# Performance work log

Hardware: AMD Instinct MI355X
Metric: run time of the kernel (lower is better)

## Reference

```python
import jax, jax.numpy as jnp
import numpy as np

MOLS = 64
ATOMS = 256
N = MOLS * ATOMS
K_GB = 32
K_GNN = 16
HID = 128
OFFSET = 0.009            # GB dielectric offset (nm)
ALPHA, BETA, GAMMA = 1.0, 0.8, 4.85  # OBC2 coefficients
EPS_FACTOR = 138.935456   # Coulomb constant, kJ*nm/(mol*e^2)
PREF = -EPS_FACTOR * (1.0 - 1.0 / 78.5)


def _edges(key, k_neigh):
    # random intra-molecule neighbors, no self loops (mimics radius-graph structure)
    src = jnp.repeat(jnp.arange(N), k_neigh)
    off = jax.random.randint(key, (N * k_neigh,), 1, ATOMS)
    dst = (src // ATOMS) * ATOMS + (src % ATOMS + off) % ATOMS
    return jnp.stack([src, dst]).astype(jnp.int32)


def setup_inputs() -> dict:
    key = jax.random.key(0)
    ks = jax.random.split(key, 8)
    pos = (jax.random.uniform(ks[0], (N, 3), jnp.float32) * 1.5)
    q = jax.random.uniform(ks[1], (N, 1), jnp.float32) - 0.5
    rad = 0.15 + 0.05 * jax.random.uniform(ks[2], (N, 1), jnp.float32)
    scl = 0.8 + 0.2 * jax.random.uniform(ks[3], (N, 1), jnp.float32)
    rest = jax.random.uniform(ks[4], (N, 4), jnp.float32)
    atom_features = jnp.concatenate([q, rad, scl, rest], axis=1)
    batch = jnp.repeat(jnp.arange(MOLS), ATOMS).astype(jnp.int32)
    edge_index = _edges(ks[5], K_GB)
    gnn_edge_index = _edges(ks[6], K_GNN)

    def lin(k, fi, fo):
        return (jax.random.normal(k, (fi, fo), jnp.float32) / np.float32(np.sqrt(fi)),
                jnp.zeros((fo,), jnp.float32))
    kw = jax.random.split(ks[7], 6)
    i1_w1, i1_b1 = lin(kw[0], 2 * 2 + 1, HID)
    i1_w2, i1_b2 = lin(kw[1], HID, HID)
    i2_w1, i2_b1 = lin(kw[2], 2 * HID + 1, HID)
    i2_w2, i2_b2 = lin(kw[3], HID, HID)
    i3_w1, i3_b1 = lin(kw[4], 2 * HID + 1, HID)
    i3_w2, i3_b2 = lin(kw[5], HID, 1)
    return dict(pos=pos, atom_features=atom_features, batch=batch,
                edge_index=edge_index, gnn_edge_index=gnn_edge_index,
                i1_w1=i1_w1, i1_b1=i1_b1, i1_w2=i1_w2, i1_b2=i1_b2,
                i2_w1=i2_w1, i2_b1=i2_b1, i2_w2=i2_w2, i2_b2=i2_b2,
                i3_w1=i3_w1, i3_b1=i3_b1, i3_w2=i3_w2, i3_b2=i3_b2)


def _dist(pos, ei):
    d2 = jnp.sum((pos[ei[0]] - pos[ei[1]]) ** 2, axis=1)
    return jnp.sqrt(d2 + 1e-12)


def _gb_energies(pos, feats, ei):
    # GBNeck_interaction (Born radii via HCT descreening integral, OBC2 rescale)
    # followed by GBNeck_energies (pairwise GB + self energy), per-atom [N,1]
    n = pos.shape[0]
    src, dst = ei[0], ei[1]
    d = _dist(pos, ei)
    q, radius, scale = feats[:, 0], feats[:, 1], feats[:, 2]
    rho = radius - OFFSET
    sr_j = (scale * rho)[src]
    rho_i = rho[dst]
    U = d + sr_j
    L = jnp.maximum(rho_i, jnp.abs(d - sr_j))
    I = 0.5 * (1.0 / L - 1.0 / U
               + 0.25 * (d - sr_j ** 2 / d) * (1.0 / U ** 2 - 1.0 / L ** 2)
               + 0.5 * jnp.log(L / U) / d)
    I = jnp.where(rho_i < U, I, 0.0)
    Isum = jax.ops.segment_sum(I, dst, num_segments=n)
    psi = Isum * rho
    B = 1.0 / (1.0 / rho - jnp.tanh(ALPHA * psi - BETA * psi ** 2 + GAMMA * psi ** 3) / radius)
    Bi, Bj = B[dst], B[src]
    f_gb = jnp.sqrt(d ** 2 + Bi * Bj * jnp.exp(-d ** 2 / (4.0 * Bi * Bj)))
    e_pair = 0.5 * PREF * q[dst] * q[src] / f_gb  # 0.5: edges are double counted
    e = 0.5 * PREF * q ** 2 / B + jax.ops.segment_sum(e_pair, dst, num_segments=n)
    return e[:, None]


def _in_layer(x, ei, d, w1, b1, w2, b2):
    # IN_layer_all_swish_2pass: edge MLP on [x_i || x_j || d] + scatter-add
    n = x.shape[0]
    m = jnp.concatenate([x[ei[0]], x[ei[1]], d[:, None]], axis=1)
    h = jax.nn.silu(m @ w1 + b1)
    return jax.ops.segment_sum(h @ w2 + b2, ei[1], num_segments=n)


def _energies_all(pos, feats, ei, gei,
                  i1_w1, i1_b1, i1_w2, i1_b2,
                  i2_w1, i2_b1, i2_w2, i2_b2,
                  i3_w1, i3_b1, i3_w2, i3_b2):
    e_gb = _gb_energies(pos, feats, ei)
    d_gnn = _dist(pos, gei)
    x = jax.nn.silu(_in_layer(feats[:, :2], gei, d_gnn, i1_w1, i1_b1, i1_w2, i1_b2))
    x = jax.nn.silu(_in_layer(x, gei, d_gnn, i2_w1, i2_b1, i2_w2, i2_b2))
    x = _in_layer(x, gei, d_gnn, i3_w1, i3_b1, i3_w2, i3_b2)
    return e_gb + x


def reference(pos, atom_features, batch, edge_index, gnn_edge_index,
              i1_w1, i1_b1, i1_w2, i1_b2,
              i2_w1, i2_b1, i2_w2, i2_b2,
              i3_w1, i3_b1, i3_w2, i3_b2):
    ws = (i1_w1, i1_b1, i1_w2, i1_b2, i2_w1, i2_b1, i2_w2, i2_b2,
          i3_w1, i3_b1, i3_w2, i3_b2)
    efun = lambda p: _energies_all(p, atom_features, edge_index, gnn_edge_index, *ws)
    energies, vjp = jax.vjp(efun, pos)  # [N,1]
    (gpos,) = vjp(jnp.ones_like(energies))
    forces = -gpos
    energy = jax.ops.segment_sum(energies[:, 0], batch, num_segments=MOLS)[:, None]
    return energy, forces
```

## Files before the change

### kernel.cpp

```cpp
#include <hip/hip_runtime.h>
#include <hip/hip_bf16.h>

#define NATOMS 16384
#define MOLS   64
#define ATOMSM 256
#define EGB    524288
#define EGNN   262144
#define HID    128
#define NH     (NATOMS*HID)

#define OFFSETC 0.009f
#define ALPHAC  1.0f
#define BETAC   0.8f
#define GAMMAC  4.85f
#define PREFC   (-138.935456f*(1.0f-1.0f/78.5f))

typedef __hip_bfloat16 bf;
typedef __attribute__((ext_vector_type(8))) short bf8v;
typedef __attribute__((ext_vector_type(4))) float f4v;

__device__ __forceinline__ float b2f(bf x){ return __bfloat162float(x); }
__device__ __forceinline__ bf f2b(float x){ return __float2bfloat16(x); }
__device__ __forceinline__ short f2s(float x){ bf h = f2b(x); return *(short*)&h; }
__device__ __forceinline__ float s2f(short s){
    unsigned int x = ((unsigned int)(unsigned short)s) << 16;
    return __uint_as_float(x);
}
__device__ __forceinline__ float sigf(float x){ return 1.0f/(1.0f+__expf(-x)); }
__device__ __forceinline__ float waveRed(float v){
    v += __shfl_xor(v,32); v += __shfl_xor(v,16); v += __shfl_xor(v,8);
    v += __shfl_xor(v,4);  v += __shfl_xor(v,2);  v += __shfl_xor(v,1);
    return v;
}

__global__ __launch_bounds__(256) void k_A(
    const float* __restrict__ A2, const float* __restrict__ C1,
    const float* __restrict__ A3, const float* __restrict__ C2,
    short* __restrict__ C1t, short* __restrict__ C2t,
    short* __restrict__ A2at, short* __restrict__ A2bt,
    short* __restrict__ A3at, short* __restrict__ A3bt,
    short* __restrict__ rA2a, short* __restrict__ rA2b,
    short* __restrict__ rA3a, short* __restrict__ rA3b,
    short* __restrict__ rC1, short* __restrict__ rC2,
    const float* __restrict__ feat, const float* __restrict__ A1,
    bf* __restrict__ u1, bf* __restrict__ v1,
    const float* __restrict__ pos, const int* __restrict__ ei,
    float* __restrict__ Isum,
    const int* __restrict__ gei, float* __restrict__ dgnn, int* __restrict__ cnt)
{
    int tid = threadIdx.x;
    if (blockIdx.x < 64){
        int gid = blockIdx.x*256 + tid;
        int j = gid >> 7, k = gid & 127;
        C1t[gid]  = f2s(C1[k*HID+j]);
        C2t[gid]  = f2s(C2[k*HID+j]);
        A2at[gid] = f2s(A2[k*HID+j]);
        A2bt[gid] = f2s(A2[(HID+k)*HID+j]);
        A3at[gid] = f2s(A3[k*HID+j]);
        A3bt[gid] = f2s(A3[(HID+k)*HID+j]);
        rA2a[gid] = f2s(A2[gid]);
        rA2b[gid] = f2s(A2[HID*HID+gid]);
        rA3a[gid] = f2s(A3[gid]);
        rA3b[gid] = f2s(A3[HID*HID+gid]);
        rC1[gid]  = f2s(C1[gid]);
        rC2[gid]  = f2s(C2[gid]);
    } else if (blockIdx.x < 4160){
        int gid2 = (blockIdx.x-64)*256 + tid;
        int i = gid2 >> 6, k2 = (gid2 & 63)*2;
        float q = feat[7*i+0], r = feat[7*i+1];
        float u0 = q*A1[k2]         + r*A1[HID+k2];
        float u1v= q*A1[k2+1]       + r*A1[HID+k2+1];
        float v0 = q*A1[2*HID+k2]   + r*A1[3*HID+k2];
        float v1v= q*A1[2*HID+k2+1] + r*A1[3*HID+k2+1];
        ushort2 uu, vv;
        uu.x = (unsigned short)f2s(u0); uu.y = (unsigned short)f2s(u1v);
        vv.x = (unsigned short)f2s(v0); vv.y = (unsigned short)f2s(v1v);
        *(ushort2*)((short*)u1 + (size_t)i*HID + k2) = uu;
        *(ushort2*)((short*)v1 + (size_t)i*HID + k2) = vv;
    } else if (blockIdx.x < 4672){
        __shared__ float sPx[256], sPy[256], sPz[256], sRho[256], sSr[256];
        __shared__ float sI[256];
        int bb = blockIdx.x - 4160;
        int mbase = (bb >> 3) * 256;
        {
            int i = mbase + tid;
            sPx[tid]=pos[3*i]; sPy[tid]=pos[3*i+1]; sPz[tid]=pos[3*i+2];
            float rad = feat[7*i+1], sc = feat[7*i+2];
            float rho = rad - OFFSETC;
            sRho[tid]=rho; sSr[tid]=sc*rho;
            sI[tid]=0.f;
        }
        __syncthreads();
        int T = bb*256 + tid;
        int s = T >> 3, p = T & 7;
        int sl = s & 255;
        int e0 = s*32 + p*4;
        float px = sPx[sl], py = sPy[sl], pz = sPz[sl];
        float sr = sSr[sl];
        const int* dP = ei + EGB;
        int4 d4 = *(const int4*)(dP + e0);
        int dls[4] = {d4.x&255, d4.y&255, d4.z&255, d4.w&255};
#pragma unroll
        for (int j=0;j<4;j++){
            int dl = dls[j];
            float dx = px - sPx[dl];
            float dy = py - sPy[dl];
            float dz = pz - sPz[dl];
            float d  = sqrtf(dx*dx+dy*dy+dz*dz + 1e-12f);
            float rho_i = sRho[dl];
            float U = d + sr;
            if (rho_i < U){
                float L = fmaxf(rho_i, fabsf(d - sr));
                float invU = 1.0f/U, invL = 1.0f/L;
                float I = 0.5f*invL - 0.5f*invU
                        + 0.125f*(d - sr*sr/d)*(invU*invU - invL*invL)
                        + 0.25f*__logf(L*invU)/d;
                atomicAdd(&sI[dl], I);
            }
        }
        __syncthreads();
        atomicAdd(&Isum[mbase + tid], sI[tid]);
    } else {
        int e = (blockIdx.x-4672)*256 + tid;
        int s = gei[e], dd = gei[EGNN+e];
        float dx = pos[3*s+0] - pos[3*dd+0];
        float dy = pos[3*s+1] - pos[3*dd+1];
        float dz = pos[3*s+2] - pos[3*dd+2];
        dgnn[e] = sqrtf(dx*dx+dy*dy+dz*dz + 1e-12f);
        atomicAdd(&cnt[dd], 1);
    }
}

__global__ __launch_bounds__(256) void k_B(
    const float* __restrict__ feat, const float* __restrict__ Isum,
    float* __restrict__ Bv, float* __restrict__ cB, float* __restrict__ gB,
    float* __restrict__ egb,
    const int* __restrict__ cnt, int* __restrict__ rptr,
    const int* __restrict__ gei, const float* __restrict__ dgnn,
    int* __restrict__ csr, int2* __restrict__ csr2)
{
    int t = threadIdx.x;
    if (blockIdx.x < 64){
        int i = blockIdx.x*256 + t;
        float q   = feat[7*i+0];
        float rad = feat[7*i+1];
        float rho = rad - OFFSETC;
        float psi = Isum[i]*rho;
        float u = psi*(ALPHAC + psi*(-BETAC + GAMMAC*psi));
        float tt = tanhf(u);
        float B = 1.0f/(1.0f/rho - tt/rad);
        Bv[i] = B;
        float du = ALPHAC + psi*(-2.0f*BETAC + 3.0f*GAMMAC*psi);
        cB[i] = B*B*((1.0f-tt*tt)/rad)*du*rho;
        float Cs = 0.5f*PREFC*q*q;
        egb[i] = Cs/B;
        gB[i]  = -Cs/(B*B);
    } else {
        __shared__ int sc[256];
        __shared__ int lcur[256];
        int m = blockIdx.x - 64;
        int c = cnt[m*256+t];
        sc[t] = c; __syncthreads();
        for (int off=1; off<256; off<<=1){
            int x = (t>=off) ? sc[t-off] : 0;
            __syncthreads();
            sc[t] += x;
            __syncthreads();
        }
        int exl = sc[t] - c;
        rptr[m*256+t] = m*4096 + exl;
        lcur[t] = exl;
        __syncthreads();
        int e0 = m*4096;
        for (int j=t; j<4096; j+=256){
            int e = e0 + j;
            int dl = gei[EGNN+e] & 255;
            float d = dgnn[e];
            int p = atomicAdd(&lcur[dl], 1);
            int idx = e0 + p;
            csr[idx] = e;
            int2 rec; rec.x = e >> 4; rec.y = __float_as_int(d);
            csr2[idx] = rec;
        }
    }
}

__global__ __launch_bounds__(256) void k_gbC(
    const float* __restrict__ pos, const float* __restrict__ feat,
    const int* __restrict__ ei, const float* __restrict__ Bv,
    float* __restrict__ egb, float* __restrict__ gdgb, float* __restrict__ gB)
{
    __shared__ float sPx[256], sPy[256], sPz[256], sB[256], sQf[256];
    __shared__ float sE[256], sG[256];
    int tid = threadIdx.x;
    int mbase = (blockIdx.x >> 3) * 256;
    {
        int i = mbase + tid;
        sPx[tid]=pos[3*i]; sPy[tid]=pos[3*i+1]; sPz[tid]=pos[3*i+2];
        sB[tid]=Bv[i]; sQf[tid]=feat[7*i+0];
        sE[tid]=0.f; sG[tid]=0.f;
    }
    __syncthreads();
    int T = blockIdx.x*256 + tid;
    int s = T >> 3, p = T & 7;
    int sl = s & 255;
    int e0 = s*32 + p*4;
    float px = sPx[sl], py = sPy[sl], pz = sPz[sl];
    float qs = sQf[sl];
    float Bs = sB[sl];
    float gsrc = 0.f;
    const int* dP = ei + EGB;
    int4 d4 = *(const int4*)(dP + e0);
    int dls[4] = {d4.x&255, d4.y&255, d4.z&255, d4.w&255};
#pragma unroll
    for (int j=0;j<4;j++){
        int dl = dls[j];
        float dx = px - sPx[dl];
        float dy = py - sPy[dl];
        float dz = pz - sPz[dl];
        float d2 = dx*dx+dy*dy+dz*dz + 1e-12f;
        float d  = sqrtf(d2);
        float Bd = sB[dl];
        float C = 0.5f*PREFC*sQf[dl]*qs;
        float P = Bd*Bs;
        float ex = __expf(-d2/(4.f*P));
        float f2 = d2 + P*ex;
        float f  = sqrtf(f2);
        float f3i = 1.f/(f2*f);
        gdgb[e0+j] = -C*d*(1.f - 0.25f*ex)*f3i;
        float common = -C*ex*(1.f + d2/(4.f*P))*0.5f*f3i;
        atomicAdd(&sE[dl], C/f);
        atomicAdd(&sG[dl], common*Bs);
        gsrc += common*Bd;
    }
    gsrc += __shfl_xor(gsrc,1);
    gsrc += __shfl_xor(gsrc,2);
    gsrc += __shfl_xor(gsrc,4);
    if (p==0) atomicAdd(&sG[sl], gsrc);
    __syncthreads();
    atomicAdd(&egb[mbase + tid], sE[tid]);
    atomicAdd(&gB[mbase + tid],  sG[tid]);
}

__global__ __launch_bounds__(256) void k_gbE(
    const float* __restrict__ pos, const float* __restrict__ feat,
    const int* __restrict__ ei, const float* __restrict__ cB,
    const float* __restrict__ gB,
    const float* __restrict__ gdgb, float* __restrict__ grad)
{
    __shared__ float sPx[256], sPy[256], sPz[256], sRho[256], sSr[256], sCg[256];
    __shared__ float sGx[256], sGy[256], sGz[256];
    int tid = threadIdx.x;
    int mbase = (blockIdx.x >> 3) * 256;
    {
        int i = mbase + tid;
        sPx[tid]=pos[3*i]; sPy[tid]=pos[3*i+1]; sPz[tid]=pos[3*i+2];
        float rad = feat[7*i+1], sc = feat[7*i+2];
        float rho = rad - OFFSETC;
        sRho[tid]=rho; sSr[tid]=sc*rho;
        sCg[tid]=cB[i]*gB[i];
        sGx[tid]=0.f; sGy[tid]=0.f; sGz[tid]=0.f;
    }
    __syncthreads();
    int T = blockIdx.x*256 + tid;
    int s = T >> 3, p = T & 7;
    int sl = s & 255;
    int e0 = s*32 + p*4;
    float px = sPx[sl], py = sPy[sl], pz = sPz[sl];
    float sr = sSr[sl];
    float gx=0.f, gy=0.f, gz=0.f;
    const int* dP = ei + EGB;
    int4 d4 = *(const int4*)(dP + e0);
    int dls[4] = {d4.x&255, d4.y&255, d4.z&255, d4.w&255};
#pragma unroll
    for (int j=0;j<4;j++){
        int dl = dls[j];
        float dx = px - sPx[dl];
        float dy = py - sPy[dl];
        float dz = pz - sPz[dl];
        float d2 = dx*dx+dy*dy+dz*dz + 1e-12f;
        float d  = sqrtf(d2);
        float rho_i = sRho[dl];
        float U = d + sr;
        float gd = gdgb[e0+j];
        if (rho_i < U){
            float aa = fabsf(d - sr);
            float L, Lp;
            if (rho_i >= aa){ L = rho_i; Lp = 0.f; }
            else { L = aa; Lp = (d >= sr) ? 1.f : -1.f; }
            float invU = 1.f/U, invL = 1.f/L;
            float invU2=invU*invU, invL2=invL*invL;
            float dIdd = -0.5f*Lp*invL2 + 0.5f*invU2
                + 0.125f*(1.f + sr*sr/d2)*(invU2 - invL2)
                + 0.125f*(d - sr*sr/d)*(2.f*Lp*invL2*invL - 2.f*invU2*invU)
                + 0.25f*((Lp*invL - invU)/d - __logf(L*invU)/d2);
            gd += sCg[dl]*dIdd;
        }
        float c = gd/d;
        gx += c*dx; gy += c*dy; gz += c*dz;
        atomicAdd(&sGx[dl], -c*dx);
        atomicAdd(&sGy[dl], -c*dy);
        atomicAdd(&sGz[dl], -c*dz);
    }
    gx += __shfl_xor(gx,1); gx += __shfl_xor(gx,2); gx += __shfl_xor(gx,4);
    gy += __shfl_xor(gy,1); gy += __shfl_xor(gy,2); gy += __shfl_xor(gy,4);
    gz += __shfl_xor(gz,1); gz += __shfl_xor(gz,2); gz += __shfl_xor(gz,4);
    if (p==0){
        atomicAdd(&sGx[sl], gx);
        atomicAdd(&sGy[sl], gy);
        atomicAdd(&sGz[sl], gz);
    }
    __syncthreads();
    int i = mbase + tid;
    atomicAdd(&grad[3*i+0], sGx[tid]);
    atomicAdd(&grad[3*i+1], sGy[tid]);
    atomicAdd(&grad[3*i+2], sGz[tid]);
}

__global__ __launch_bounds__(128) void k_edge_fwd_dst(
    const int2* __restrict__ csr2, const int* __restrict__ rptr, const int* __restrict__ cnt,
    const bf* __restrict__ u, const bf* __restrict__ v,
    const float* __restrict__ wdp, const float* __restrict__ bb,
    bf* __restrict__ Hs, bf* __restrict__ Sds)
{
    __shared__ int2 se[128];
    int dst = blockIdx.x, k = threadIdx.x;
    int n = cnt[dst], r0 = rptr[dst];
    int nn = n < 128 ? n : 128;
    if (k < nn) se[k] = csr2[r0+k];
    __syncthreads();
    float wd = wdp[k];
    float base = b2f(v[dst*HID+k]) + bb[k];
    const short* usk = (const short*)u + k;
    float hsum = 0.f, dssum = 0.f;
#pragma unroll 4
    for (int j=0;j<nn;j++){
        int2 rec = se[j];
        float a = s2f(usk[(size_t)rec.x*HID]) + base + __int_as_float(rec.y)*wd;
        float sg = sigf(a);
        hsum += a*sg;
        dssum += sg*(1.f + a*(1.f - sg));
    }
    for (int j=128;j<n;j++){
        int2 rec = csr2[r0+j];
        float a = s2f(usk[(size_t)rec.x*HID]) + base + __int_as_float(rec.y)*wd;
        float sg = sigf(a);
        hsum += a*sg;
        dssum += sg*(1.f + a*(1.f - sg));
    }
    Hs[dst*HID+k] = f2b(hsum);
    if (Sds) Sds[dst*HID+k] = f2b(dssum);
}

__global__ __launch_bounds__(256) void k_node_fwd_uv_mfma(
    const short* __restrict__ Hs, const int* __restrict__ cnt,
    const short* __restrict__ Ct, const float* __restrict__ D,
    const short* __restrict__ Aat, const short* __restrict__ Abt,
    bf* __restrict__ dsz, bf* __restrict__ u, bf* __restrict__ v)
{
    __shared__ short sx[64*HID];
    int lane = threadIdx.x & 63, w = threadIdx.x >> 6;
    int m0 = blockIdx.x*64 + w*16;
    int ar = lane & 15, kg = lane >> 4;
    bf8v af[4];
#pragma unroll
    for (int s=0;s<4;s++) af[s] = *(const bf8v*)&Hs[(size_t)(m0+ar)*HID + s*32 + kg*8];
    f4v acc[8];
#pragma unroll
    for (int nt=0;nt<8;nt++){
        acc[nt] = (f4v){0.f,0.f,0.f,0.f};
        const short* bp = Ct + (nt*16+ar)*HID + kg*8;
#pragma unroll
        for (int s=0;s<4;s++){
            bf8v bv = *(const bf8v*)(bp + s*32);
            acc[nt] = __builtin_amdgcn_mfma_f32_16x16x32_bf16(af[s], bv, acc[nt], 0,0,0);
        }
    }
    float cn[4];
#pragma unroll
    for (int r=0;r<4;r++) cn[r] = (float)cnt[m0 + kg*4 + r];
#pragma unroll
    for (int nt=0;nt<8;nt++){
        int j = nt*16 + ar;
        float Dj = D[j];
#pragma unroll
        for (int r=0;r<4;r++){
            int m = m0 + kg*4 + r;
            float zv = acc[nt][r] + cn[r]*Dj;
            float sg = sigf(zv);
            dsz[(size_t)m*HID + j] = f2b(sg*(1.f + zv*(1.f - sg)));
            sx[(w*16 + kg*4 + r)*HID + j] = f2s(zv*sg);
        }
    }
    __syncthreads();
#pragma unroll
    for (int s=0;s<4;s++) af[s] = *(const bf8v*)&sx[(w*16+ar)*HID + s*32 + kg*8];
    f4v au[8], av[8];
#pragma unroll
    for (int nt=0;nt<8;nt++){
        au[nt] = (f4v){0.f,0.f,0.f,0.f};
        av[nt] = (f4v){0.f,0.f,0.f,0.f};
        const short* bpa = Aat + (nt*16+ar)*HID + kg*8;
        const short* bpb = Abt + (nt*16+ar)*HID + kg*8;
#pragma unroll
        for (int s=0;s<4;s++){
            bf8v ba = *(const bf8v*)(bpa + s*32);
            bf8v bb = *(const bf8v*)(bpb + s*32);
            au[nt] = __builtin_amdgcn_mfma_f32_16x16x32_bf16(af[s], ba, au[nt], 0,0,0);
            av[nt] = __builtin_amdgcn_mfma_f32_16x16x32_bf16(af[s], bb, av[nt], 0,0,0);
        }
    }
#pragma unroll
    for (int nt=0;nt<8;nt++){
        int j = nt*16 + ar;
#pragma unroll
        for (int r=0;r<4;r++){
            int m = m0 + kg*4 + r;
            u[(size_t)m*HID + j] = f2b(au[nt][r]);
            v[(size_t)m*HID + j] = f2b(av[nt][r]);
        }
    }
}

__global__ __launch_bounds__(256) void k_gx_node_bwd_mfma(
    const short* __restrict__ Gs, const short* __restrict__ Gd,
    const short* __restrict__ gHin, const short* __restrict__ Sds,
    const short* __restrict__ Ra, const short* __restrict__ Rb,
    const bf* __restrict__ dsz, const short* __restrict__ Rc,
    bf* __restrict__ gHout)
{
    __shared__ short st[64*HID];
    int lane = threadIdx.x & 63, w = threadIdx.x >> 6;
    int m0 = blockIdx.x*64 + w*16;
    int ar = lane & 15, kg = lane >> 4;
    bf8v as_[4], ad_[4];
#pragma unroll
    for (int s=0;s<4;s++)
        as_[s] = *(const bf8v*)&Gs[(size_t)(m0+ar)*HID + s*32 + kg*8];
    if (Sds){
#pragma unroll
        for (int s=0;s<4;s++){
            bf8v g = *(const bf8v*)&gHin[(size_t)(m0+ar)*HID + s*32 + kg*8];
            bf8v sd = *(const bf8v*)&Sds[(size_t)(m0+ar)*HID + s*32 + kg*8];
            bf8v r;
#pragma unroll
            for (int i=0;i<8;i++) r[i] = f2s(s2f(g[i])*s2f(sd[i]));
            ad_[s] = r;
        }
    } else {
#pragma unroll
        for (int s=0;s<4;s++)
            ad_[s] = *(const bf8v*)&Gd[(size_t)(m0+ar)*HID + s*32 + kg*8];
    }
    f4v acc[8];
#pragma unroll
    for (int nt=0;nt<8;nt++){
        acc[nt] = (f4v){0.f,0.f,0.f,0.f};
        const short* bpa = Ra + (nt*16+ar)*HID + kg*8;
        const short* bpb = Rb + (nt*16+ar)*HID + kg*8;
#pragma unroll
        for (int s=0;s<4;s++){
            bf8v ba = *(const bf8v*)(bpa + s*32);
            bf8v bb = *(const bf8v*)(bpb + s*32);
            acc[nt] = __builtin_amdgcn_mfma_f32_16x16x32_bf16(as_[s], ba, acc[nt], 0,0,0);
            acc[nt] = __builtin_amdgcn_mfma_f32_16x16x32_bf16(ad_[s], bb, acc[nt], 0,0,0);
        }
    }
#pragma unroll
    for (int nt=0;nt<8;nt++){
        int j = nt*16 + ar;
#pragma unroll
        for (int r=0;r<4;r++){
            int m = m0 + kg*4 + r;
            float t = acc[nt][r] * b2f(dsz[(size_t)m*HID + j]);
            st[(w*16 + kg*4 + r)*HID + j] = f2s(t);
        }
    }
    __syncthreads();
    bf8v af[4];
#pragma unroll
    for (int s=0;s<4;s++) af[s] = *(const bf8v*)&st[(w*16+ar)*HID + s*32 + kg*8];
    f4v a2[8];
#pragma unroll
    for (int nt=0;nt<8;nt++){
        a2[nt] = (f4v){0.f,0.f,0.f,0.f};
        const short* bp = Rc + (nt*16+ar)*HID + kg*8;
#pragma unroll
        for (int s=0;s<4;s++){
            bf8v bc = *(const bf8v*)(bp + s*32);
            a2[nt] = __builtin_amdgcn_mfma_f32_16x16x32_bf16(af[s], bc, a2[nt], 0,0,0);
        }
    }
#pragma unroll
    for (int nt=0;nt<8;nt++){
        int j = nt*16 + ar;
#pragma unroll
        for (int r=0;r<4;r++){
            gHout[(size_t)(m0 + kg*4 + r)*HID + j] = f2b(a2[nt][r]);
        }
    }
}

__global__ __launch_bounds__(128) void k_l3(
    const int2* __restrict__ csr2, const int* __restrict__ rptr, const int* __restrict__ cnt,
    const int* __restrict__ gei, const float* __restrict__ dgnn,
    const bf* __restrict__ u, const bf* __restrict__ v,
    const float* __restrict__ A3, const float* __restrict__ B3,
    const float* __restrict__ C3, const float* __restrict__ D3,
    bf* __restrict__ Gd, float* __restrict__ x3,
    bf* __restrict__ Gs, float* __restrict__ gdg)
{
    int k = threadIdx.x;
    if (blockIdx.x < NATOMS){
        __shared__ float rr[2];
        __shared__ int2 se[128];
        int dst = blockIdx.x;
        int n = cnt[dst], r0 = rptr[dst];
        int nn = n < 128 ? n : 128;
        if (k < nn) se[k] = csr2[r0+k];
        __syncthreads();
        float wd = A3[256*HID+k], ck = C3[k];
        float base = b2f(v[dst*HID+k]) + B3[k];
        const short* usk = (const short*)u + k;
        float hsum = 0.f, dssum = 0.f;
#pragma unroll 4
        for (int j=0;j<nn;j++){
            int2 rec = se[j];
            float a = s2f(usk[(size_t)rec.x*HID]) + base + __int_as_float(rec.y)*wd;
            float sg = sigf(a);
            hsum += a*sg;
            dssum += sg*(1.f + a*(1.f - sg));
        }
        for (int j=128;j<n;j++){
            int2 rec = csr2[r0+j];
            float a = s2f(usk[(size_t)rec.x*HID]) + base + __int_as_float(rec.y)*wd;
            float sg = sigf(a);
            hsum += a*sg;
            dssum += sg*(1.f + a*(1.f - sg));
        }
        Gd[dst*HID+k] = f2b(ck*dssum);
        float pv = waveRed(ck*hsum);
        if ((k&63)==0) rr[k>>6] = pv;
        __syncthreads();
        if (k==0) x3[dst] = rr[0] + rr[1] + (float)n*D3[0];
    } else {
        __shared__ short sv[2048];
        __shared__ float sQ[16][130];
        __shared__ float sd[16];
        int s = blockIdx.x - NATOMS;
        {
            int t = k >> 3, q = k & 7;
            int dst = gei[EGNN + s*16 + t];
            const bf8v* vr = (const bf8v*)((const short*)v + (size_t)dst*HID);
            ((bf8v*)sv)[t*16 + q*2]     = vr[q*2];
            ((bf8v*)sv)[t*16 + q*2 + 1] = vr[q*2+1];
        }
        if (k < 16) sd[k] = dgnn[s*16+k];
        __syncthreads();
        float wd = A3[256*HID+k], ck = C3[k];
        float ub = s2f(((const short*)u)[(size_t)s*HID+k]) + B3[k];
        float cw = ck*wd;
        float gs = 0.f;
#pragma unroll
        for (int t=0;t<16;t++){
            float a = ub + s2f(sv[t*128+k]) + sd[t]*wd;
            float sg = sigf(a);
            float dv = sg*(1.f + a*(1.f - sg));
            gs += dv;
            sQ[t][k] = dv*cw;
        }
        Gs[s*HID+k] = f2b(ck*gs);
        __syncthreads();
        int t = k >> 3, r = k & 7;
        float pg = 0.f;
#pragma unroll
        for (int i=0;i<16;i++) pg += sQ[t][i + 16*r];
        pg += __shfl_xor(pg,1); pg += __shfl_xor(pg,2); pg += __shfl_xor(pg,4);
        if (r==0) gdg[s*16+t] = pg;
    }
}

__global__ __launch_bounds__(128) void k_bwd_src(
    const int* __restrict__ gei, const float* __restrict__ dgnn,
    const bf* __restrict__ u, const bf* __restrict__ v,
    const float* __restrict__ wdp, const float* __restrict__ bb,
    const bf* __restrict__ gH,
    bf* __restrict__ Gs, float* __restrict__ gdg)
{
    __shared__ short sv[2048];
    __shared__ short sgh[2048];
    __shared__ float sQ[16][130];
    __shared__ float sd[16];
    int s = blockIdx.x, k = threadIdx.x;
    {
        int t = k >> 3, q = k & 7;
        int dst = gei[EGNN + s*16 + t];
        const bf8v* vr = (const bf8v*)((const short*)v + (size_t)dst*HID);
        const bf8v* gr = (const bf8v*)((const short*)gH + (size_t)dst*HID);
        ((bf8v*)sv)[t*16 + q*2]      = vr[q*2];
        ((bf8v*)sv)[t*16 + q*2 + 1]  = vr[q*2+1];
        ((bf8v*)sgh)[t*16 + q*2]     = gr[q*2];
        ((bf8v*)sgh)[t*16 + q*2 + 1] = gr[q*2+1];
    }
    if (k < 16) sd[k] = dgnn[s*16+k];
    __syncthreads();
    float wd = wdp[k];
    float ub = s2f(((const short*)u)[(size_t)s*HID+k]) + bb[k];
    float gs = 0.f;
#pragma unroll
    for (int t=0;t<16;t++){
        float a = ub + s2f(sv[t*128+k]) + sd[t]*wd;
        float sg = sigf(a);
        float dv = sg*(1.f + a*(1.f - sg));
        float ga = s2f(sgh[t*128+k]) * dv;
        gs += ga;
        sQ[t][k] = ga*wd;
    }
    Gs[s*HID+k] = f2b(gs);
    __syncthreads();
    int t = k >> 3, r = k & 7;
    float pg = 0.f;
#pragma unroll
    for (int i=0;i<16;i++) pg += sQ[t][i + 16*r];
    pg += __shfl_xor(pg,1); pg += __shfl_xor(pg,2); pg += __shfl_xor(pg,4);
    if (r==0) gdg[s*16+t] += pg;
}

__global__ __launch_bounds__(128) void k_bwd1_src(
    const int* __restrict__ gei, const float* __restrict__ dgnn,
    const bf* __restrict__ u, const bf* __restrict__ v,
    const float* __restrict__ wdp, const float* __restrict__ bb,
    const bf* __restrict__ gH,
    float* __restrict__ gdg)
{
    __shared__ short sv[2048];
    __shared__ short sgh[2048];
    __shared__ float sQ[16][130];
    __shared__ float sd[16];
    int s = blockIdx.x, k = threadIdx.x;
    {
        int t = k >> 3, q = k & 7;
        int dst = gei[EGNN + s*16 + t];
        const bf8v* vr = (const bf8v*)((const short*)v + (size_t)dst*HID);
        const bf8v* gr = (const bf8v*)((const short*)gH + (size_t)dst*HID);
        ((bf8v*)sv)[t*16 + q*2]      = vr[q*2];
        ((bf8v*)sv)[t*16 + q*2 + 1]  = vr[q*2+1];
        ((bf8v*)sgh)[t*16 + q*2]     = gr[q*2];
        ((bf8v*)sgh)[t*16 + q*2 + 1] = gr[q*2+1];
    }
    if (k < 16) sd[k] = dgnn[s*16+k];
    __syncthreads();
    float wd = wdp[k];
    float ub = s2f(((const short*)u)[(size_t)s*HID+k]) + bb[k];
#pragma unroll
    for (int t=0;t<16;t++){
        float a = ub + s2f(sv[t*128+k]) + sd[t]*wd;
        float sg = sigf(a);
        float dv = sg*(1.f + a*(1.f - sg));
        float ga = s2f(sgh[t*128+k]) * dv;
        sQ[t][k] = ga*wd;
    }
    __syncthreads();
    int t = k >> 3, r = k & 7;
    float pg = 0.f;
#pragma unroll
    for (int i=0;i<16;i++) pg += sQ[t][i + 16*r];
    pg += __shfl_xor(pg,1); pg += __shfl_xor(pg,2); pg += __shfl_xor(pg,4);
    if (r==0) gdg[s*16+t] += pg;
}

__global__ __launch_bounds__(256) void k_out(
    const float* __restrict__ pos, const int* __restrict__ gei,
    const int* __restrict__ csr, const int* __restrict__ rptr, const int* __restrict__ cnt,
    const float* __restrict__ dgnn, const float* __restrict__ gdg,
    const float* __restrict__ grad,
    const float* __restrict__ egb, const float* __restrict__ x3,
    float* __restrict__ out)
{
    int tid = threadIdx.x;
    if (blockIdx.x < 512){
        float* fout = out + MOLS;
        int T = blockIdx.x*256 + tid;
        int i = T >> 3, p = T & 7;
        float px = pos[3*i+0], py = pos[3*i+1], pz = pos[3*i+2];
        float ax=0.f, ay=0.f, az=0.f;
        for (int j=p;j<16;j+=8){
            int e = i*16 + j;
            int o = gei[EGNN+e];
            float c = gdg[e]/dgnn[e];
            ax += c*(px - pos[3*o+0]);
            ay += c*(py - pos[3*o+1]);
            az += c*(pz - pos[3*o+2]);
        }
        int n = cnt[i], r0 = rptr[i];
        for (int j=p;j<n;j+=8){
            int e = csr[r0+j];
            int o = e >> 4;
            float c = gdg[e]/dgnn[e];
            ax += c*(px - pos[3*o+0]);
            ay += c*(py - pos[3*o+1]);
            az += c*(pz - pos[3*o+2]);
        }
        ax += __shfl_xor(ax,1); ax += __shfl_xor(ax,2); ax += __shfl_xor(ax,4);
        ay += __shfl_xor(ay,1); ay += __shfl_xor(ay,2); ay += __shfl_xor(ay,4);
        az += __shfl_xor(az,1); az += __shfl_xor(az,2); az += __shfl_xor(az,4);
        if (p==0){
            fout[3*i+0] = -(grad[3*i+0] + ax);
            fout[3*i+1] = -(grad[3*i+1] + ay);
            fout[3*i+2] = -(grad[3*i+2] + az);
        }
    } else {
        __shared__ float red[4];
        int m = blockIdx.x - 512;
        int i = m*ATOMSM + tid;
        float en = egb[i] + x3[i];
        float v = waveRed(en);
        int wave = tid>>6, lane = tid&63;
        if (lane==0) red[wave] = v;
        __syncthreads();
        if (tid==0) out[m] = red[0]+red[1]+red[2]+red[3];
    }
}

extern "C" void kernel_launch(void* const* d_in, const int* in_sizes, int n_in,
                              void* d_out, int out_size, void* d_ws, size_t ws_size,
                              hipStream_t stream)
{
    const float* pos  = (const float*)d_in[0];
    const float* feat = (const float*)d_in[1];
    const int* ei  = (const int*)d_in[3];
    const int* gei = (const int*)d_in[4];
    const float* A1f = (const float*)d_in[5];  const float* B1f = (const float*)d_in[6];
    const float* C1f = (const float*)d_in[7];  const float* D1f = (const float*)d_in[8];
    const float* A2f = (const float*)d_in[9];  const float* B2f = (const float*)d_in[10];
    const float* C2f = (const float*)d_in[11]; const float* D2f = (const float*)d_in[12];
    const float* A3f = (const float*)d_in[13]; const float* B3f = (const float*)d_in[14];
    const float* C3f = (const float*)d_in[15]; const float* D3f = (const float*)d_in[16];

    float* w = (float*)d_ws;
    size_t off = 0;
    auto nxt = [&](size_t n)->float*{ float* p = w + off; off += (n + 255) & ~(size_t)255; return p; };
    float* Isum = nxt(NATOMS);
    int*   cnt  = (int*)nxt(NATOMS);
    float* grad = nxt(3*NATOMS);
    float* Bv = nxt(NATOMS); float* cB = nxt(NATOMS);
    float* gB = nxt(NATOMS); float* egb = nxt(NATOMS); float* x3 = nxt(NATOMS);
    int*   rptr = (int*)nxt(NATOMS);
    int*   csr  = (int*)nxt(EGNN);
    int2*  csr2 = (int2*)nxt((size_t)EGNN*2);
    float* dgnn = nxt(EGNN); float* gdgnn = nxt(EGNN); float* gdgb = nxt(EGB);
    bf* dsz1 = (bf*)nxt(NH/2); bf* dsz2 = (bf*)nxt(NH/2);
    bf* Hs1 = (bf*)nxt(NH/2); bf* Hs2 = (bf*)nxt(NH/2);
    bf* Gs3 = (bf*)nxt(NH/2); bf* Gd3 = (bf*)nxt(NH/2);
    bf* Sds2 = (bf*)nxt(NH/2);
    bf* u1 = (bf*)nxt(NH/2); bf* v1 = (bf*)nxt(NH/2);
    bf* u2 = (bf*)nxt(NH/2); bf* v2 = (bf*)nxt(NH/2);
    bf* v3 = (bf*)nxt(NH/2);
    short* C1t  = (short*)nxt(8192); short* C2t  = (short*)nxt(8192);
    short* A2at = (short*)nxt(8192); short* A2bt = (short*)nxt(8192);
    short* A3at = (short*)nxt(8192); short* A3bt = (short*)nxt(8192);
    short* rA2a = (short*)nxt(8192); short* rA2b = (short*)nxt(8192);
    short* rA3a = (short*)nxt(8192); short* rA3b = (short*)nxt(8192);
    short* rC1  = (short*)nxt(8192); short* rC2  = (short*)nxt(8192);
    bf* u3  = Hs1;
    bf* gH2 = Hs2;
    bf* Gs2 = Gs3;
    bf* gH1 = u3;

    hipMemsetAsync(Isum, 0, (size_t)5*NATOMS*sizeof(float), stream);

    k_A<<<64 + NH/512 + 512 + EGNN/256, 256, 0, stream>>>(
        A2f, C1f, A3f, C2f,
        C1t, C2t, A2at, A2bt, A3at, A3bt, rA2a, rA2b, rA3a, rA3b, rC1, rC2,
        feat, A1f, u1, v1,
        pos, ei, Isum, gei, dgnn, cnt);

    k_B<<<128,256,0,stream>>>(feat, Isum, Bv, cB, gB, egb, cnt, rptr,
                              gei, dgnn, csr, csr2);
    k_gbC<<<512,256,0,stream>>>(pos, feat, ei, Bv, egb, gdgb, gB);
    k_gbE<<<512,256,0,stream>>>(pos, feat, ei, cB, gB, gdgb, grad);

    k_edge_fwd_dst<<<NATOMS,128,0,stream>>>(csr2, rptr, cnt, u1, v1,
                                            A1f+4*HID, B1f, Hs1, (bf*)nullptr);
    k_node_fwd_uv_mfma<<<NATOMS/64,256,0,stream>>>((const short*)Hs1, cnt, C1t, D1f,
                                                   A2at, A2bt, dsz1, u2, v2);
    k_edge_fwd_dst<<<NATOMS,128,0,stream>>>(csr2, rptr, cnt, u2, v2,
                                            A2f+256*HID, B2f, Hs2, Sds2);
    k_node_fwd_uv_mfma<<<NATOMS/64,256,0,stream>>>((const short*)Hs2, cnt, C2t, D2f,
                                                   A3at, A3bt, dsz2, u3, v3);

    k_l3<<<2*NATOMS,128,0,stream>>>(csr2, rptr, cnt, gei, dgnn, u3, v3,
                                    A3f, B3f, C3f, D3f, Gd3, x3, Gs3, gdgnn);

    k_gx_node_bwd_mfma<<<NATOMS/64,256,0,stream>>>((const short*)Gs3, (const short*)Gd3,
        (const short*)nullptr, (const short*)nullptr, rA3a, rA3b, dsz2, rC2, gH2);
    k_bwd_src<<<NATOMS,128,0,stream>>>(gei, dgnn, u2, v2, A2f+256*HID, B2f, gH2, Gs2, gdgnn);
    k_gx_node_bwd_mfma<<<NATOMS/64,256,0,stream>>>((const short*)Gs2, (const short*)nullptr,
        (const short*)gH2, (const short*)Sds2, rA2a, rA2b, dsz1, rC1, gH1);
    k_bwd1_src<<<NATOMS,128,0,stream>>>(gei, dgnn, u1, v1, A1f+4*HID, B1f, gH1, gdgnn);

    k_out<<<576,256,0,stream>>>(pos, gei, csr, rptr, cnt, dgnn, gdgnn,
                                grad, egb, x3, (float*)d_out);
}
```

Baseline: 373.0 us.

## Process GNN edges one node per wavefront with packed bf16 pairs and readlane broadcast

The per-edge forward, layer-3 and backward-source kernels now assign one 64-lane wavefront per node instead of a 128-thread block. Each lane handles two hidden channels read as a packed bf16 pair, and edge records are broadcast with readlane instead of being staged in shared memory with barriers. Per-edge weight-gradient reductions become wave shuffles, replacing the shared-memory transpose reductions, and the two backward-source kernels are merged into one. Launch order is also shuffled so the GB kernels sit between GNN stages, which may give some overlap. This trades some register pressure and serialized readlane loops for fewer barriers, less LDS traffic and fewer, wider blocks.

```diff
diff --git a/kernel.cpp b/kernel.cpp
--- a/kernel.cpp
+++ b/kernel.cpp
@@ -18,6 +18,7 @@
 typedef __hip_bfloat16 bf;
 typedef __attribute__((ext_vector_type(8))) short bf8v;
 typedef __attribute__((ext_vector_type(4))) float f4v;
+typedef unsigned int uint;
 
 __device__ __forceinline__ float b2f(bf x){ return __bfloat162float(x); }
 __device__ __forceinline__ bf f2b(float x){ return __float2bfloat16(x); }
@@ -32,6 +33,11 @@
     v += __shfl_xor(v,4);  v += __shfl_xor(v,2);  v += __shfl_xor(v,1);
     return v;
 }
+__device__ __forceinline__ uint pack2(float a, float b){
+    return (uint)(unsigned short)f2s(a) | ((uint)(unsigned short)f2s(b) << 16);
+}
+__device__ __forceinline__ float lo2f(uint w){ return __uint_as_float(w << 16); }
+__device__ __forceinline__ float hi2f(uint w){ return __uint_as_float(w & 0xffff0000u); }
 
 __global__ __launch_bounds__(256) void k_A(
     const float* __restrict__ A2, const float* __restrict__ C1,
@@ -179,7 +185,8 @@
             int p = atomicAdd(&lcur[dl], 1);
             int idx = e0 + p;
             csr[idx] = e;
-            int2 rec; rec.x = e >> 4; rec.y = __float_as_int(d);
+            int2 rec; rec.x = (e >> 4) << 8;
+            rec.y = __float_as_int(d);
             csr2[idx] = rec;
         }
     }
@@ -317,39 +324,172 @@
     atomicAdd(&grad[3*i+2], sGz[tid]);
 }
 
-__global__ __launch_bounds__(128) void k_edge_fwd_dst(
+
+__device__ __forceinline__ void edge_fwd_wave(
+    int dst, int lane,
     const int2* __restrict__ csr2, const int* __restrict__ rptr, const int* __restrict__ cnt,
-    const bf* __restrict__ u, const bf* __restrict__ v,
+    const uint* __restrict__ u, const uint* __restrict__ v,
     const float* __restrict__ wdp, const float* __restrict__ bb,
-    bf* __restrict__ Hs, bf* __restrict__ Sds)
-{
-    __shared__ int2 se[128];
-    int dst = blockIdx.x, k = threadIdx.x;
+    uint* __restrict__ Hs, uint* __restrict__ Sds)
+{
     int n = cnt[dst], r0 = rptr[dst];
-    int nn = n < 128 ? n : 128;
-    if (k < nn) se[k] = csr2[r0+k];
-    __syncthreads();
-    float wd = wdp[k];
-    float base = b2f(v[dst*HID+k]) + bb[k];
-    const short* usk = (const short*)u + k;
-    float hsum = 0.f, dssum = 0.f;
-#pragma unroll 4
-    for (int j=0;j<nn;j++){
-        int2 rec = se[j];
-        float a = s2f(usk[(size_t)rec.x*HID]) + base + __int_as_float(rec.y)*wd;
-        float sg = sigf(a);
-        hsum += a*sg;
-        dssum += sg*(1.f + a*(1.f - sg));
-    }
-    for (int j=128;j<n;j++){
-        int2 rec = csr2[r0+j];
-        float a = s2f(usk[(size_t)rec.x*HID]) + base + __int_as_float(rec.y)*wd;
-        float sg = sigf(a);
-        hsum += a*sg;
-        dssum += sg*(1.f + a*(1.f - sg));
-    }
-    Hs[dst*HID+k] = f2b(hsum);
-    if (Sds) Sds[dst*HID+k] = f2b(dssum);
+    float2 wd = *(const float2*)&wdp[2*lane];
+    float2 b2 = *(const float2*)&bb[2*lane];
+    uint vp = v[dst*64 + lane];
+    float base0 = lo2f(vp) + b2.x;
+    float base1 = hi2f(vp) + b2.y;
+    float h0=0.f,h1=0.f,e0a=0.f,e1a=0.f;
+    for (int j0=0; j0<n; j0+=64){
+        int m = n - j0; if (m > 64) m = 64;
+        int rx = 0, ry = 0;
+        if (lane < m){ int2 rc = csr2[r0+j0+lane]; rx = rc.x; ry = rc.y; }
+#pragma unroll 2
+        for (int j=0;j<m;j++){
+            int off = __builtin_amdgcn_readlane(rx, j);
+            float d  = __uint_as_float((unsigned)__builtin_amdgcn_readlane(ry, j));
+            uint up = *(const uint*)((const char*)u + off + 4*lane);
+            float a0 = fmaf(d, wd.x, base0 + lo2f(up));
+            float a1 = fmaf(d, wd.y, base1 + hi2f(up));
+            float s0 = sigf(a0), s1 = sigf(a1);
+            float p0 = a0*s0, p1 = a1*s1;
+            h0 += p0; h1 += p1;
+            e0a = fmaf(s0, 1.f + a0 - p0, e0a);
+            e1a = fmaf(s1, 1.f + a1 - p1, e1a);
+        }
+    }
+    Hs[dst*64+lane] = pack2(h0,h1);
+    if (Sds) Sds[dst*64+lane] = pack2(e0a,e1a);
+}
+
+__global__ __launch_bounds__(256,8) void k_edge_fwd(
+    const int2* __restrict__ csr2, const int* __restrict__ rptr, const int* __restrict__ cnt,
+    const uint* __restrict__ u, const uint* __restrict__ v,
+    const float* __restrict__ wdp, const float* __restrict__ bb,
+    uint* __restrict__ Hs, uint* __restrict__ Sds)
+{
+    int lane = threadIdx.x & 63, wid = threadIdx.x >> 6;
+    int dst = blockIdx.x*4 + wid;
+    edge_fwd_wave(dst, lane, csr2, rptr, cnt, u, v, wdp, bb, Hs, Sds);
+}
+
+__global__ __launch_bounds__(256,8) void k_l3(
+    const int2* __restrict__ csr2, const int* __restrict__ rptr, const int* __restrict__ cnt,
+    const int* __restrict__ gei, const float* __restrict__ dgnn,
+    const uint* __restrict__ u, const uint* __restrict__ v,
+    const float* __restrict__ A3, const float* __restrict__ B3,
+    const float* __restrict__ C3, const float* __restrict__ D3,
+    uint* __restrict__ Gd, float* __restrict__ x3,
+    uint* __restrict__ Gs, float* __restrict__ gdg)
+{
+    int lane = threadIdx.x & 63, wid = threadIdx.x >> 6;
+    const float* wdp = A3 + 256*HID;
+    if (blockIdx.x < NATOMS/4){
+        int dst = blockIdx.x*4 + wid;
+        int n = cnt[dst], r0 = rptr[dst];
+        float2 wd = *(const float2*)&wdp[2*lane];
+        float2 b2 = *(const float2*)&B3[2*lane];
+        float2 ck = *(const float2*)&C3[2*lane];
+        uint vp = v[dst*64 + lane];
+        float base0 = lo2f(vp) + b2.x;
+        float base1 = hi2f(vp) + b2.y;
+        float h0=0.f,h1=0.f,e0a=0.f,e1a=0.f;
+        for (int j0=0; j0<n; j0+=64){
+            int m = n - j0; if (m > 64) m = 64;
+            int rx = 0, ry = 0;
+            if (lane < m){ int2 rc = csr2[r0+j0+lane]; rx = rc.x; ry = rc.y; }
+#pragma unroll 2
+            for (int j=0;j<m;j++){
+                int off = __builtin_amdgcn_readlane(rx, j);
+                float d  = __uint_as_float((unsigned)__builtin_amdgcn_readlane(ry, j));
+                uint up = *(const uint*)((const char*)u + off + 4*lane);
+                float a0 = fmaf(d, wd.x, base0 + lo2f(up));
+                float a1 = fmaf(d, wd.y, base1 + hi2f(up));
+                float s0 = sigf(a0), s1 = sigf(a1);
+                float p0 = a0*s0, p1 = a1*s1;
+                h0 += p0; h1 += p1;
+                e0a = fmaf(s0, 1.f + a0 - p0, e0a);
+                e1a = fmaf(s1, 1.f + a1 - p1, e1a);
+            }
+        }
+        Gd[dst*64+lane] = pack2(ck.x*e0a, ck.y*e1a);
+        float px = waveRed(ck.x*h0 + ck.y*h1);
+        if (lane==0) x3[dst] = px + (float)n*D3[0];
+    } else {
+        int s = (blockIdx.x - NATOMS/4)*4 + wid;
+        int doff = 0, dbit = 0;
+        if (lane < 16){
+            doff = gei[EGNN + s*16 + lane] << 8;
+            dbit = __float_as_int(dgnn[s*16+lane]);
+        }
+        float2 wd = *(const float2*)&wdp[2*lane];
+        float2 b2 = *(const float2*)&B3[2*lane];
+        float2 ck = *(const float2*)&C3[2*lane];
+        uint up = u[s*64 + lane];
+        float us0 = lo2f(up) + b2.x;
+        float us1 = hi2f(up) + b2.y;
+        float cw0 = ck.x*wd.x, cw1 = ck.y*wd.y;
+        float gs0=0.f, gs1=0.f, acc=0.f;
+#pragma unroll
+        for (int t=0;t<16;t++){
+            int off = __builtin_amdgcn_readlane(doff, t);
+            float d = __uint_as_float((unsigned)__builtin_amdgcn_readlane(dbit, t));
+            uint vp = *(const uint*)((const char*)v + off + 4*lane);
+            float a0 = fmaf(d, wd.x, us0 + lo2f(vp));
+            float a1 = fmaf(d, wd.y, us1 + hi2f(vp));
+            float s0 = sigf(a0), s1 = sigf(a1);
+            float p0 = a0*s0, p1 = a1*s1;
+            float dv0 = s0*(1.f + a0 - p0);
+            float dv1 = s1*(1.f + a1 - p1);
+            gs0 += dv0; gs1 += dv1;
+            float pg = fmaf(dv1, cw1, dv0*cw0);
+            pg = waveRed(pg);
+            acc = (lane==t) ? pg : acc;
+        }
+        Gs[s*64+lane] = pack2(ck.x*gs0, ck.y*gs1);
+        if (lane < 16) gdg[s*16+lane] = acc;
+    }
+}
+
+__global__ __launch_bounds__(256,8) void k_bwd_src(
+    const int* __restrict__ gei, const float* __restrict__ dgnn,
+    const uint* __restrict__ u, const uint* __restrict__ v,
+    const float* __restrict__ wdp, const float* __restrict__ bb,
+    const uint* __restrict__ gH,
+    uint* __restrict__ Gs, float* __restrict__ gdg)
+{
+    int lane = threadIdx.x & 63, wid = threadIdx.x >> 6;
+    int s = blockIdx.x*4 + wid;
+    int doff = 0, dbit = 0; float gold = 0.f;
+    if (lane < 16){
+        doff = gei[EGNN + s*16 + lane] << 8;
+        dbit = __float_as_int(dgnn[s*16+lane]);
+        gold = gdg[s*16+lane];
+    }
+    float2 wd = *(const float2*)&wdp[2*lane];
+    float2 b2 = *(const float2*)&bb[2*lane];
+    uint up = u[s*64 + lane];
+    float us0 = lo2f(up) + b2.x;
+    float us1 = hi2f(up) + b2.y;
+    float gs0=0.f, gs1=0.f, acc=0.f;
+#pragma unroll
+    for (int t=0;t<16;t++){
+        int off = __builtin_amdgcn_readlane(doff, t);
+        float d = __uint_as_float((unsigned)__builtin_amdgcn_readlane(dbit, t));
+        uint vp = *(const uint*)((const char*)v + off + 4*lane);
+        uint gp = *(const uint*)((const char*)gH + off + 4*lane);
+        float a0 = fmaf(d, wd.x, us0 + lo2f(vp));
+        float a1 = fmaf(d, wd.y, us1 + hi2f(vp));
+        float s0 = sigf(a0), s1 = sigf(a1);
+        float p0 = a0*s0, p1 = a1*s1;
+        float ga0 = s0*(1.f + a0 - p0) * lo2f(gp);
+        float ga1 = s1*(1.f + a1 - p1) * hi2f(gp);
+        gs0 += ga0; gs1 += ga1;
+        float pg = fmaf(ga1, wd.y, ga0*wd.x);
+        pg = waveRed(pg);
+        acc = (lane==t) ? pg : acc;
+    }
+    if (Gs) Gs[s*64+lane] = pack2(gs0, gs1);
+    if (lane < 16) gdg[s*16+lane] = gold + acc;
 }
 
 __global__ __launch_bounds__(256) void k_node_fwd_uv_mfma(
@@ -499,174 +639,6 @@
             gHout[(size_t)(m0 + kg*4 + r)*HID + j] = f2b(a2[nt][r]);
         }
     }
-}
-
-__global__ __launch_bounds__(128) void k_l3(
-    const int2* __restrict__ csr2, const int* __restrict__ rptr, const int* __restrict__ cnt,
-    const int* __restrict__ gei, const float* __restrict__ dgnn,
-    const bf* __restrict__ u, const bf* __restrict__ v,
-    const float* __restrict__ A3, const float* __restrict__ B3,
-    const float* __restrict__ C3, const float* __restrict__ D3,
-    bf* __restrict__ Gd, float* __restrict__ x3,
-    bf* __restrict__ Gs, float* __restrict__ gdg)
-{
-    int k = threadIdx.x;
-    if (blockIdx.x < NATOMS){
-        __shared__ float rr[2];
-        __shared__ int2 se[128];
-        int dst = blockIdx.x;
-        int n = cnt[dst], r0 = rptr[dst];
-        int nn = n < 128 ? n : 128;
-        if (k < nn) se[k] = csr2[r0+k];
-        __syncthreads();
-        float wd = A3[256*HID+k], ck = C3[k];
-        float base = b2f(v[dst*HID+k]) + B3[k];
-        const short* usk = (const short*)u + k;
-        float hsum = 0.f, dssum = 0.f;
-#pragma unroll 4
-        for (int j=0;j<nn;j++){
-            int2 rec = se[j];
-            float a = s2f(usk[(size_t)rec.x*HID]) + base + __int_as_float(rec.y)*wd;
-            float sg = sigf(a);
-            hsum += a*sg;
-            dssum += sg*(1.f + a*(1.f - sg));
-        }
-        for (int j=128;j<n;j++){
-            int2 rec = csr2[r0+j];
-            float a = s2f(usk[(size_t)rec.x*HID]) + base + __int_as_float(rec.y)*wd;
-            float sg = sigf(a);
-            hsum += a*sg;
-            dssum += sg*(1.f + a*(1.f - sg));
-        }
-        Gd[dst*HID+k] = f2b(ck*dssum);
-        float pv = waveRed(ck*hsum);
-        if ((k&63)==0) rr[k>>6] = pv;
-        __syncthreads();
-        if (k==0) x3[dst] = rr[0] + rr[1] + (float)n*D3[0];
-    } else {
-        __shared__ short sv[2048];
-        __shared__ float sQ[16][130];
-        __shared__ float sd[16];
-        int s = blockIdx.x - NATOMS;
-        {
-            int t = k >> 3, q = k & 7;
-            int dst = gei[EGNN + s*16 + t];
-            const bf8v* vr = (const bf8v*)((const short*)v + (size_t)dst*HID);
-            ((bf8v*)sv)[t*16 + q*2]     = vr[q*2];
-            ((bf8v*)sv)[t*16 + q*2 + 1] = vr[q*2+1];
-        }
-        if (k < 16) sd[k] = dgnn[s*16+k];
-        __syncthreads();
-        float wd = A3[256*HID+k], ck = C3[k];
-        float ub = s2f(((const short*)u)[(size_t)s*HID+k]) + B3[k];
-        float cw = ck*wd;
-        float gs = 0.f;
-#pragma unroll
-        for (int t=0;t<16;t++){
-            float a = ub + s2f(sv[t*128+k]) + sd[t]*wd;
-            float sg = sigf(a);
-            float dv = sg*(1.f + a*(1.f - sg));
-            gs += dv;
-            sQ[t][k] = dv*cw;
-        }
-        Gs[s*HID+k] = f2b(ck*gs);
-        __syncthreads();
-        int t = k >> 3, r = k & 7;
-        float pg = 0.f;
-#pragma unroll
-        for (int i=0;i<16;i++) pg += sQ[t][i + 16*r];
-        pg += __shfl_xor(pg,1); pg += __shfl_xor(pg,2); pg += __shfl_xor(pg,4);
-        if (r==0) gdg[s*16+t] = pg;
-    }
-}
-
-__global__ __launch_bounds__(128) void k_bwd_src(
-    const int* __restrict__ gei, const float* __restrict__ dgnn,
-    const bf* __restrict__ u, const bf* __restrict__ v,
-    const float* __restrict__ wdp, const float* __restrict__ bb,
-    const bf* __restrict__ gH,
-    bf* __restrict__ Gs, float* __restrict__ gdg)
-{
-    __shared__ short sv[2048];
-    __shared__ short sgh[2048];
-    __shared__ float sQ[16][130];
-    __shared__ float sd[16];
-    int s = blockIdx.x, k = threadIdx.x;
-    {
-        int t = k >> 3, q = k & 7;
-        int dst = gei[EGNN + s*16 + t];
-        const bf8v* vr = (const bf8v*)((const short*)v + (size_t)dst*HID);
-        const bf8v* gr = (const bf8v*)((const short*)gH + (size_t)dst*HID);
-        ((bf8v*)sv)[t*16 + q*2]      = vr[q*2];
-        ((bf8v*)sv)[t*16 + q*2 + 1]  = vr[q*2+1];
-        ((bf8v*)sgh)[t*16 + q*2]     = gr[q*2];
-        ((bf8v*)sgh)[t*16 + q*2 + 1] = gr[q*2+1];
-    }
-    if (k < 16) sd[k] = dgnn[s*16+k];
-    __syncthreads();
-    float wd = wdp[k];
-    float ub = s2f(((const short*)u)[(size_t)s*HID+k]) + bb[k];
-    float gs = 0.f;
-#pragma unroll
-    for (int t=0;t<16;t++){
-        float a = ub + s2f(sv[t*128+k]) + sd[t]*wd;
-        float sg = sigf(a);
-        float dv = sg*(1.f + a*(1.f - sg));
-        float ga = s2f(sgh[t*128+k]) * dv;
-        gs += ga;
-        sQ[t][k] = ga*wd;
-    }
-    Gs[s*HID+k] = f2b(gs);
-    __syncthreads();
-    int t = k >> 3, r = k & 7;
-    float pg = 0.f;
-#pragma unroll
-    for (int i=0;i<16;i++) pg += sQ[t][i + 16*r];
-    pg += __shfl_xor(pg,1); pg += __shfl_xor(pg,2); pg += __shfl_xor(pg,4);
-    if (r==0) gdg[s*16+t] += pg;
-}
-
-__global__ __launch_bounds__(128) void k_bwd1_src(
-    const int* __restrict__ gei, const float* __restrict__ dgnn,
-    const bf* __restrict__ u, const bf* __restrict__ v,
-    const float* __restrict__ wdp, const float* __restrict__ bb,
-    const bf* __restrict__ gH,
-    float* __restrict__ gdg)
-{
-    __shared__ short sv[2048];
-    __shared__ short sgh[2048];
-    __shared__ float sQ[16][130];
-    __shared__ float sd[16];
-    int s = blockIdx.x, k = threadIdx.x;
-    {
-        int t = k >> 3, q = k & 7;
-        int dst = gei[EGNN + s*16 + t];
-        const bf8v* vr = (const bf8v*)((const short*)v + (size_t)dst*HID);
-        const bf8v* gr = (const bf8v*)((const short*)gH + (size_t)dst*HID);
-        ((bf8v*)sv)[t*16 + q*2]      = vr[q*2];
-        ((bf8v*)sv)[t*16 + q*2 + 1]  = vr[q*2+1];
-        ((bf8v*)sgh)[t*16 + q*2]     = gr[q*2];
-        ((bf8v*)sgh)[t*16 + q*2 + 1] = gr[q*2+1];
-    }
-    if (k < 16) sd[k] = dgnn[s*16+k];
-    __syncthreads();
-    float wd = wdp[k];
-    float ub = s2f(((const short*)u)[(size_t)s*HID+k]) + bb[k];
-#pragma unroll
-    for (int t=0;t<16;t++){
-        float a = ub + s2f(sv[t*128+k]) + sd[t]*wd;
-        float sg = sigf(a);
-        float dv = sg*(1.f + a*(1.f - sg));
-        float ga = s2f(sgh[t*128+k]) * dv;
-        sQ[t][k] = ga*wd;
-    }
-    __syncthreads();
-    int t = k >> 3, r = k & 7;
-    float pg = 0.f;
-#pragma unroll
-    for (int i=0;i<16;i++) pg += sQ[t][i + 16*r];
-    pg += __shfl_xor(pg,1); pg += __shfl_xor(pg,2); pg += __shfl_xor(pg,4);
-    if (r==0) gdg[s*16+t] += pg;
 }
 
 __global__ __launch_bounds__(256) void k_out(
@@ -777,27 +749,33 @@
 
     k_B<<<128,256,0,stream>>>(feat, Isum, Bv, cB, gB, egb, cnt, rptr,
                               gei, dgnn, csr, csr2);
+
+    k_edge_fwd<<<NATOMS/4,256,0,stream>>>(csr2, rptr, cnt, (const uint*)u1, (const uint*)v1,
+                                          A1f+4*HID, B1f, (uint*)Hs1, (uint*)nullptr);
     k_gbC<<<512,256,0,stream>>>(pos, feat, ei, Bv, egb, gdgb, gB);
-    k_gbE<<<512,256,0,stream>>>(pos, feat, ei, cB, gB, gdgb, grad);
-
-    k_edge_fwd_dst<<<NATOMS,128,0,stream>>>(csr2, rptr, cnt, u1, v1,
-                                            A1f+4*HID, B1f, Hs1, (bf*)nullptr);
     k_node_fwd_uv_mfma<<<NATOMS/64,256,0,stream>>>((const short*)Hs1, cnt, C1t, D1f,
                                                    A2at, A2bt, dsz1, u2, v2);
-    k_edge_fwd_dst<<<NATOMS,128,0,stream>>>(csr2, rptr, cnt, u2, v2,
-                                            A2f+256*HID, B2f, Hs2, Sds2);
+    k_edge_fwd<<<NATOMS/4,256,0,stream>>>(csr2, rptr, cnt, (const uint*)u2, (const uint*)v2,
+                                          A2f+256*HID, B2f, (uint*)Hs2, (uint*)Sds2);
+    k_gbE<<<512,256,0,stream>>>(pos, feat, ei, cB, gB, gdgb, grad);
     k_node_fwd_uv_mfma<<<NATOMS/64,256,0,stream>>>((const short*)Hs2, cnt, C2t, D2f,
                                                    A3at, A3bt, dsz2, u3, v3);
 
-    k_l3<<<2*NATOMS,128,0,stream>>>(csr2, rptr, cnt, gei, dgnn, u3, v3,
-                                    A3f, B3f, C3f, D3f, Gd3, x3, Gs3, gdgnn);
+    k_l3<<<2*(NATOMS/4),256,0,stream>>>(csr2, rptr, cnt, gei, dgnn,
+                                        (const uint*)u3, (const uint*)v3,
+                                        A3f, B3f, C3f, D3f,
+                                        (uint*)Gd3, x3, (uint*)Gs3, gdgnn);
 
     k_gx_node_bwd_mfma<<<NATOMS/64,256,0,stream>>>((const short*)Gs3, (const short*)Gd3,
         (const short*)nullptr, (const short*)nullptr, rA3a, rA3b, dsz2, rC2, gH2);
-    k_bwd_src<<<NATOMS,128,0,stream>>>(gei, dgnn, u2, v2, A2f+256*HID, B2f, gH2, Gs2, gdgnn);
+    k_bwd_src<<<NATOMS/4,256,0,stream>>>(gei, dgnn, (const uint*)u2, (const uint*)v2,
+                                         A2f+256*HID, B2f, (const uint*)gH2,
+                                         (uint*)Gs2, gdgnn);
     k_gx_node_bwd_mfma<<<NATOMS/64,256,0,stream>>>((const short*)Gs2, (const short*)nullptr,
         (const short*)gH2, (const short*)Sds2, rA2a, rA2b, dsz1, rC1, gH1);
-    k_bwd1_src<<<NATOMS,128,0,stream>>>(gei, dgnn, u1, v1, A1f+4*HID, B1f, gH1, gdgnn);
+    k_bwd_src<<<NATOMS/4,256,0,stream>>>(gei, dgnn, (const uint*)u1, (const uint*)v1,
+                                         A1f+4*HID, B1f, (const uint*)gH1,
+                                         (uint*)nullptr, gdgnn);
 
     k_out<<<576,256,0,stream>>>(pos, gei, csr, rptr, cnt, dgnn, gdgnn,
                                 grad, egb, x3, (float*)d_out);
```

Result: slower. 410.4 us (+10.0%).
